# Kernel optimization log

Hardware: AMD Instinct MI355X
Metric: run time of the kernel (lower is better)

The kernel has to match this reference:

```python
import jax, jax.numpy as jnp
import numpy as np

EPS = 1e-5
H, DH = 8, 8  # n_head, d_hidden


def setup_inputs() -> dict:
    key = jax.random.key(0)
    ks = jax.random.split(key, 6)
    B, N, L, D = 1, 512, 1024, 64
    s = 1.0 / np.sqrt(D)
    return {
        "msa": jax.random.normal(ks[0], (B, N, L, D), jnp.float32),
        "ln_w": jnp.ones((D,), jnp.float32),
        "ln_b": jnp.zeros((D,), jnp.float32),
        "Wq": jax.random.normal(ks[1], (D, H * DH), jnp.float32) * s,
        "Wk": jax.random.normal(ks[2], (D, DH), jnp.float32) * s,
        "Wv": jax.random.normal(ks[3], (D, DH), jnp.float32) * s,
        "Wg": jax.random.normal(ks[4], (D, H * DH), jnp.float32) * s,
        "bg": jnp.ones((H * DH,), jnp.float32),
        "Wout": jax.random.normal(ks[5], (D, D), jnp.float32) * s,
        "bout": jnp.zeros((D,), jnp.float32),
    }


def reference(msa, ln_w, ln_b, Wq, Wk, Wv, Wg, bg, Wout, bout):
    B, N, L, D = msa.shape
    # LayerNorm over d_msa
    mu = jnp.mean(msa, axis=-1, keepdims=True)
    var = jnp.mean(jnp.square(msa - mu), axis=-1, keepdims=True)
    x = (msa - mu) * jax.lax.rsqrt(var + EPS) * ln_w + ln_b

    # Global query: project, split heads, mean over the N (sequence) axis
    q = (x @ Wq).reshape(B, N, L, H, DH).mean(axis=1)  # (B, L, H, DH)
    k = x @ Wk  # (B, N, L, DH)
    v = x @ Wv  # (B, N, L, DH)
    gate = jax.nn.sigmoid(x @ Wg + bg)  # (B, N, L, H*DH)

    scale = 1.0 / np.sqrt(DH)
    # SDPA batched over (B, L): q_len = H, kv_len = N, head_dim = DH
    scores = jnp.einsum("blhd,bnld->blhn", q, k) * scale
    attn = jax.nn.softmax(scores, axis=-1)
    o = jnp.einsum("blhn,bnld->blhd", attn, v)  # (B, L, H, DH)
    o = o.reshape(B, 1, L, H * DH)  # broadcast over N via gate

    out = (gate * o) @ Wout + bout  # (B, N, L, D)
    return out
```

## Files before the change

### kernel.cpp

```cpp
#include <hip/hip_runtime.h>
#include <math.h>

#define DD 64
#define NN 512
#define LL 1024
#define EPSF 1e-5f
#define NCH 32

typedef short short8 __attribute__((ext_vector_type(8)));
typedef float f32x4 __attribute__((ext_vector_type(4)));

static __device__ __forceinline__ unsigned bf16_rne(float f) {
  unsigned u = __float_as_uint(f);
  return (u + 0x7FFFu + ((u >> 16) & 1u)) >> 16;
}
static __device__ __forceinline__ float bf16_hi_f(float f) {
  unsigned u = __float_as_uint(f);
  return __uint_as_float((u + 0x7FFFu + ((u >> 16) & 1u)) & 0xFFFF0000u);
}

__global__ __launch_bounds__(256) void kW(const float* __restrict__ Wg,
                                          const float* __restrict__ Wout,
                                          unsigned* __restrict__ Bpk)
{
  const int idx = blockIdx.x * 256 + threadIdx.x;
  const int e2   = idx & 3;
  const int lane = (idx >> 2) & 63;
  const int ctkt = (idx >> 8) & 7;
  const int h    = (idx >> 11) & 1;
  const int mv   = (idx >> 12) & 1;
  const int col  = ((ctkt >> 1) << 4) | (lane & 15);
  const int k0   = ((ctkt & 1) << 5) + ((lane >> 4) << 3) + (e2 << 1);
  const float* W = mv ? Wout : Wg;
  const float w0 = W[k0 * DD + col];
  const float w1 = W[(k0 + 1) * DD + col];
  unsigned b0, b1;
  if (h == 0) { b0 = bf16_rne(w0); b1 = bf16_rne(w1); }
  else        { b0 = bf16_rne(w0 - bf16_hi_f(w0)); b1 = bf16_rne(w1 - bf16_hi_f(w1)); }
  Bpk[idx] = b0 | (b1 << 16);
}

__global__ __launch_bounds__(256, 4) void kA(
    const float* __restrict__ msa, const float* __restrict__ lnw, const float* __restrict__ lnb,
    const float* __restrict__ Wk, const float* __restrict__ Wv,
    float* __restrict__ kb, float* __restrict__ vb, float* __restrict__ xbarP)
{
  __shared__ float xc[4][16][68];
  const int t = threadIdx.x;
  const int lane = t & 63;
  const int w = t >> 6;
  const int l_loc = t & 15;
  const int n_loc = t >> 4;
  const int lt = blockIdx.x & 63;
  const int nc = blockIdx.x >> 6;
  const int l0 = lt * 16;
  const int n = nc * 16 + n_loc;
  const int l = l0 + l_loc;

  float X[DD];
  {
    const float4* rp = (const float4*)(msa + ((size_t)n * LL + l) * DD);
#pragma unroll
    for (int i = 0; i < 16; ++i) {
      const float4 f = rp[i];
      X[4*i+0] = f.x; X[4*i+1] = f.y; X[4*i+2] = f.z; X[4*i+3] = f.w;
    }
  }

  float s = 0.f, s2 = 0.f;
#pragma unroll
  for (int d = 0; d < DD; ++d) { s += X[d]; s2 = fmaf(X[d], X[d], s2); }
  const float mu = s * (1.f / DD);
  const float rs = rsqrtf(fmaf(-mu, mu, s2 * (1.f / DD)) + EPSF);

  float ka[8], va[8];
#pragma unroll
  for (int j = 0; j < 8; ++j) { ka[j] = 0.f; va[j] = 0.f; }
#pragma unroll
  for (int d = 0; d < DD; ++d) {
    const float xn = fmaf((X[d] - mu) * rs, lnw[d], lnb[d]);
    X[d] = xn;
#pragma unroll
    for (int j = 0; j < 8; ++j) {
      ka[j] = fmaf(xn, Wk[d * 8 + j], ka[j]);
      va[j] = fmaf(xn, Wv[d * 8 + j], va[j]);
    }
  }

  {
    float4* kp = (float4*)(kb + ((size_t)l * NN + n) * 8);
    float4* vp = (float4*)(vb + ((size_t)l * NN + n) * 8);
    kp[0] = make_float4(ka[0], ka[1], ka[2], ka[3]);
    kp[1] = make_float4(ka[4], ka[5], ka[6], ka[7]);
    vp[0] = make_float4(va[0], va[1], va[2], va[3]);
    vp[1] = make_float4(va[4], va[5], va[6], va[7]);
  }

  {
    const bool hi1 = (lane & 16) != 0;
#pragma unroll
    for (int k = 0; k < 32; ++k) {
      const float keep = hi1 ? X[k + 32] : X[k];
      const float send = hi1 ? X[k] : X[k + 32];
      X[k] = keep + __shfl_xor(send, 16);
    }
    const bool hi2 = (lane & 32) != 0;
#pragma unroll
    for (int k = 0; k < 16; ++k) {
      const float keep = hi2 ? X[k + 16] : X[k];
      const float send = hi2 ? X[k] : X[k + 16];
      X[k] = keep + __shfl_xor(send, 32);
    }
  }
  const int d0 = ((lane >> 4) & 1) * 32 + (lane >> 5) * 16;
#pragma unroll
  for (int k = 0; k < 16; ++k) xc[w][l_loc][d0 + k] = X[k];
  __syncthreads();

#pragma unroll
  for (int j = 0; j < 4; ++j) {
    const int c = t * 4 + j;
    const int ll = c >> 6, d = c & 63;
    const float sv = xc[0][ll][d] + xc[1][ll][d] + xc[2][ll][d] + xc[3][ll][d];
    xbarP[((size_t)(l0 + ll) * NCH + nc) * DD + d] = sv;
  }
}

__global__ __launch_bounds__(512) void kB(
    const float* __restrict__ kb, const float* __restrict__ vb,
    const float* __restrict__ xbarP, const float* __restrict__ Wq,
    float* __restrict__ ob)
{
  __shared__ float xbL[DD];
  __shared__ float qs[DD];
  __shared__ float ks[NN * 9];
  __shared__ float vs[NN * 9];
  const int l = blockIdx.x;
  const int t = threadIdx.x;
  const int h = t >> 6;
  const int lane = t & 63;

  const float* kl = kb + (size_t)l * NN * 8;
  const float* vl = vb + (size_t)l * NN * 8;
#pragma unroll
  for (int i = 0; i < 8; ++i) {
    const int idx = i * 512 + t;
    const int n = idx >> 3, j = idx & 7;
    ks[n*9 + j] = kl[idx];
    vs[n*9 + j] = vl[idx];
  }
  if (t < DD) {
    float s = 0.f;
    for (int p = 0; p < NCH; ++p) s += xbarP[((size_t)l * NCH + p) * DD + t];
    xbL[t] = s * (1.f / NN);
  }
  __syncthreads();
  if (t < DD) {
    float acc = 0.f;
    for (int d = 0; d < DD; ++d) acc = fmaf(xbL[d], Wq[d*DD + t], acc);
    qs[t] = acc * 0.35355339059327373f;
  }
  __syncthreads();

  float sc[8];
  float m = -1e30f;
#pragma unroll
  for (int i = 0; i < 8; ++i) {
    const int n = i * 64 + lane;
    float s = 0.f;
#pragma unroll
    for (int d = 0; d < 8; ++d) s = fmaf(qs[h*8 + d], ks[n*9 + d], s);
    sc[i] = s;
    m = fmaxf(m, s);
  }
#pragma unroll
  for (int off = 32; off; off >>= 1) m = fmaxf(m, __shfl_xor(m, off));
  float ssum = 0.f;
#pragma unroll
  for (int i = 0; i < 8; ++i) { sc[i] = __expf(sc[i] - m); ssum += sc[i]; }
#pragma unroll
  for (int off = 32; off; off >>= 1) ssum += __shfl_xor(ssum, off);
  const float inv = 1.f / ssum;

  float oacc[8];
#pragma unroll
  for (int d = 0; d < 8; ++d) oacc[d] = 0.f;
#pragma unroll
  for (int i = 0; i < 8; ++i) {
    const int n = i * 64 + lane;
#pragma unroll
    for (int d = 0; d < 8; ++d) oacc[d] = fmaf(sc[i], vs[n*9 + d], oacc[d]);
  }
#pragma unroll
  for (int d = 0; d < 8; ++d) {
#pragma unroll
    for (int off = 32; off; off >>= 1) oacc[d] += __shfl_xor(oacc[d], off);
  }
  if (lane == 0) {
    float4* op = (float4*)(ob + (size_t)l * DD + h * 8);
    op[0] = make_float4(oacc[0]*inv, oacc[1]*inv, oacc[2]*inv, oacc[3]*inv);
    op[1] = make_float4(oacc[4]*inv, oacc[5]*inv, oacc[6]*inv, oacc[7]*inv);
  }
}

__global__ __launch_bounds__(256, 4) void kC(
    const float* __restrict__ msa, const float* __restrict__ lnw, const float* __restrict__ lnb,
    const unsigned* __restrict__ Bpk, const float* __restrict__ bg,
    const float* __restrict__ ob, const float* __restrict__ bout,
    float* __restrict__ out)
{
  __shared__ unsigned Bl[4096];
  __shared__ unsigned short XH[128 * 72];
  __shared__ unsigned short XL[128 * 72];
  const int t = threadIdx.x;
  const int lane = t & 63;
  const int w = t >> 6;
  const int rbase = 32 * w;
  const size_t R0 = (size_t)blockIdx.x * 128;

#pragma unroll
  for (int i = 0; i < 16; ++i) Bl[i * 256 + t] = Bpk[i * 256 + t];

  if (t < 128) {
    const float4* rp = (const float4*)(msa + (R0 + t) * DD);
    float4 r4[16];
#pragma unroll
    for (int i = 0; i < 16; ++i) r4[i] = rp[i];
    float s = 0.f, s2 = 0.f;
#pragma unroll
    for (int i = 0; i < 16; ++i) {
      const float4 f = r4[i];
      s += (f.x + f.y) + (f.z + f.w);
      s2 = fmaf(f.x, f.x, s2); s2 = fmaf(f.y, f.y, s2);
      s2 = fmaf(f.z, f.z, s2); s2 = fmaf(f.w, f.w, s2);
    }
    const float mu = s * (1.f / DD);
    const float rs = rsqrtf(fmaf(-mu, mu, s2 * (1.f / DD)) + EPSF);
    const float aa = rs, bb = -mu * rs;
#pragma unroll
    for (int i = 0; i < 16; ++i) {
      const float xs0 = r4[i].x, xs1 = r4[i].y, xs2 = r4[i].z, xs3 = r4[i].w;
      unsigned hh[4], ll[4];
#define XN_SPLIT(c, xv)                                               \
      {                                                               \
        const int d = 4 * i + (c);                                    \
        const float xn = fmaf(fmaf((xv), aa, bb), lnw[d], lnb[d]);    \
        const float hf = bf16_hi_f(xn);                               \
        hh[c] = bf16_rne(xn);                                         \
        ll[c] = bf16_rne(xn - hf);                                    \
      }
      XN_SPLIT(0, xs0) XN_SPLIT(1, xs1) XN_SPLIT(2, xs2) XN_SPLIT(3, xs3)
#undef XN_SPLIT
      *(uint2*)&XH[t * 72 + 4 * i] = make_uint2(hh[0] | (hh[1] << 16), hh[2] | (hh[3] << 16));
      *(uint2*)&XL[t * 72 + 4 * i] = make_uint2(ll[0] | (ll[1] << 16), ll[2] | (ll[3] << 16));
    }
  }
  __syncthreads();

  auto run_mv = [&](f32x4 acc[2][4]) {
#pragma unroll
    for (int rt = 0; rt < 2; ++rt) {
      const int row = rbase + rt * 16 + (lane & 15);
      const int kg = (lane >> 4) * 8;
      const short8 ah0 = *(const short8*)&XH[row * 72 + kg];
      const short8 ah1 = *(const short8*)&XH[row * 72 + 32 + kg];
      const short8 al0 = *(const short8*)&XL[row * 72 + kg];
      const short8 al1 = *(const short8*)&XL[row * 72 + 32 + kg];
#pragma unroll
      for (int ct = 0; ct < 4; ++ct) {
        const short8 bh0 = *(const short8*)&Bl[((0 * 8 + ct * 2 + 0) * 64 + lane) * 4];
        const short8 bh1 = *(const short8*)&Bl[((0 * 8 + ct * 2 + 1) * 64 + lane) * 4];
        const short8 bl0 = *(const short8*)&Bl[((1 * 8 + ct * 2 + 0) * 64 + lane) * 4];
        const short8 bl1 = *(const short8*)&Bl[((1 * 8 + ct * 2 + 1) * 64 + lane) * 4];
        f32x4 c = acc[rt][ct];
        c = __builtin_amdgcn_mfma_f32_16x16x32_bf16(ah0, bh0, c, 0, 0, 0);
        c = __builtin_amdgcn_mfma_f32_16x16x32_bf16(ah1, bh1, c, 0, 0, 0);
        c = __builtin_amdgcn_mfma_f32_16x16x32_bf16(ah0, bl0, c, 0, 0, 0);
        c = __builtin_amdgcn_mfma_f32_16x16x32_bf16(ah1, bl1, c, 0, 0, 0);
        c = __builtin_amdgcn_mfma_f32_16x16x32_bf16(al0, bh0, c, 0, 0, 0);
        c = __builtin_amdgcn_mfma_f32_16x16x32_bf16(al1, bh1, c, 0, 0, 0);
        acc[rt][ct] = c;
      }
    }
  };

  f32x4 acc[2][4];
#pragma unroll
  for (int rt = 0; rt < 2; ++rt)
#pragma unroll
    for (int ct = 0; ct < 4; ++ct) acc[rt][ct] = f32x4{0.f, 0.f, 0.f, 0.f};
  run_mv(acc);

#pragma unroll
  for (int rt = 0; rt < 2; ++rt) {
    const int rl0 = rbase + rt * 16 + ((lane >> 4) << 2);
#pragma unroll
    for (int ct = 0; ct < 4; ++ct) {
      const int col = ct * 16 + (lane & 15);
      const float bgc = bg[col];
#pragma unroll
      for (int j = 0; j < 4; ++j) {
        const int rl = rl0 + j;
        const int li = (int)((R0 + rl) & (LL - 1));
        const float o = ob[(size_t)li * DD + col];
        const float pre = acc[rt][ct][j] + bgc;
        const float tv = o / (1.f + __expf(-pre));
        const float hf = bf16_hi_f(tv);
        XH[rl * 72 + col] = (unsigned short)bf16_rne(tv);
        XL[rl * 72 + col] = (unsigned short)bf16_rne(tv - hf);
      }
    }
  }
  __syncthreads();

#pragma unroll
  for (int i = 0; i < 16; ++i) Bl[i * 256 + t] = Bpk[4096 + i * 256 + t];
  __syncthreads();

#pragma unroll
  for (int rt = 0; rt < 2; ++rt)
#pragma unroll
    for (int ct = 0; ct < 4; ++ct) {
      const float bo = bout[ct * 16 + (lane & 15)];
      acc[rt][ct] = f32x4{bo, bo, bo, bo};
    }
  run_mv(acc);

#pragma unroll
  for (int rt = 0; rt < 2; ++rt) {
#pragma unroll
    for (int j = 0; j < 4; ++j) {
      const size_t rg = R0 + rbase + rt * 16 + ((lane >> 4) << 2) + j;
#pragma unroll
      for (int ct = 0; ct < 4; ++ct)
        out[rg * DD + ct * 16 + (lane & 15)] = acc[rt][ct][j];
    }
  }
}

extern "C" void kernel_launch(void* const* d_in, const int* in_sizes, int n_in,
                              void* d_out, int out_size, void* d_ws, size_t ws_size,
                              hipStream_t stream)
{
  const float* msa  = (const float*)d_in[0];
  const float* lnw  = (const float*)d_in[1];
  const float* lnb  = (const float*)d_in[2];
  const float* Wq   = (const float*)d_in[3];
  const float* Wk   = (const float*)d_in[4];
  const float* Wv   = (const float*)d_in[5];
  const float* Wg   = (const float*)d_in[6];
  const float* bg   = (const float*)d_in[7];
  const float* Wout = (const float*)d_in[8];
  const float* bout = (const float*)d_in[9];
  float* out = (float*)d_out;

  float* kb    = (float*)d_ws;
  float* vb    = kb + (size_t)LL * NN * 8;
  float* xbarP = vb + (size_t)LL * NN * 8;
  float* ob    = xbarP + (size_t)LL * NCH * DD;
  unsigned* Bpk = (unsigned*)(ob + (size_t)LL * DD);

  kW<<<32, 256, 0, stream>>>(Wg, Wout, Bpk);
  kA<<<64 * NCH, 256, 0, stream>>>(msa, lnw, lnb, Wk, Wv, kb, vb, xbarP);
  kB<<<LL, 512, 0, stream>>>(kb, vb, xbarP, Wq, ob);
  kC<<<(NN * LL) / 128, 256, 0, stream>>>(msa, lnw, lnb, Bpk, bg, ob, bout, out);
}
```

Before: 141.6 us.

## Drop LDS weight staging and block barriers in gated output kernel

The fused gate/output kernel now reads packed bf16 weight fragments straight from global memory (cached) instead of staging them in shared memory. That removes the 16 KB LDS buffer and all three block-wide barriers, since each wave only touches its own rows of the normalized-activation tile. LayerNorm is split across all 256 threads, two per row, combined with a shuffle. The attention output is stored transposed so each lane gets its four row values with one float4 load, and the MFMA loop is reordered so each weight fragment is reused across both row tiles. The risks are more global/L1 traffic for weight fragments and reliance on wave-local LDS ordering for correctness.

Result: faster. 134.1 us (-5.3%).

```diff
diff --git a/kernel.cpp b/kernel.cpp
--- a/kernel.cpp
+++ b/kernel.cpp
@@ -129,7 +129,7 @@
 __global__ __launch_bounds__(512) void kB(
     const float* __restrict__ kb, const float* __restrict__ vb,
     const float* __restrict__ xbarP, const float* __restrict__ Wq,
-    float* __restrict__ ob)
+    float* __restrict__ obT)
 {
   __shared__ float xbL[DD];
   __shared__ float qs[DD];
@@ -197,19 +197,18 @@
     for (int off = 32; off; off >>= 1) oacc[d] += __shfl_xor(oacc[d], off);
   }
   if (lane == 0) {
-    float4* op = (float4*)(ob + (size_t)l * DD + h * 8);
-    op[0] = make_float4(oacc[0]*inv, oacc[1]*inv, oacc[2]*inv, oacc[3]*inv);
-    op[1] = make_float4(oacc[4]*inv, oacc[5]*inv, oacc[6]*inv, oacc[7]*inv);
+#pragma unroll
+    for (int d = 0; d < 8; ++d)
+      obT[(size_t)(h * 8 + d) * LL + l] = oacc[d] * inv;
   }
 }
 
 __global__ __launch_bounds__(256, 4) void kC(
     const float* __restrict__ msa, const float* __restrict__ lnw, const float* __restrict__ lnb,
     const unsigned* __restrict__ Bpk, const float* __restrict__ bg,
-    const float* __restrict__ ob, const float* __restrict__ bout,
+    const float* __restrict__ obT, const float* __restrict__ bout,
     float* __restrict__ out)
 {
-  __shared__ unsigned Bl[4096];
   __shared__ unsigned short XH[128 * 72];
   __shared__ unsigned short XL[128 * 72];
   const int t = threadIdx.x;
@@ -217,33 +216,34 @@
   const int w = t >> 6;
   const int rbase = 32 * w;
   const size_t R0 = (size_t)blockIdx.x * 128;
-
-#pragma unroll
-  for (int i = 0; i < 16; ++i) Bl[i * 256 + t] = Bpk[i * 256 + t];
-
-  if (t < 128) {
-    const float4* rp = (const float4*)(msa + (R0 + t) * DD);
-    float4 r4[16];
-#pragma unroll
-    for (int i = 0; i < 16; ++i) r4[i] = rp[i];
+  const int row = t >> 1;
+  const int half = t & 1;
+
+  {
+    const float4* rp = (const float4*)(msa + (R0 + row) * DD + half * 32);
+    float4 r4[8];
+#pragma unroll
+    for (int i = 0; i < 8; ++i) r4[i] = rp[i];
     float s = 0.f, s2 = 0.f;
 #pragma unroll
-    for (int i = 0; i < 16; ++i) {
+    for (int i = 0; i < 8; ++i) {
       const float4 f = r4[i];
       s += (f.x + f.y) + (f.z + f.w);
       s2 = fmaf(f.x, f.x, s2); s2 = fmaf(f.y, f.y, s2);
       s2 = fmaf(f.z, f.z, s2); s2 = fmaf(f.w, f.w, s2);
     }
+    s += __shfl_xor(s, 1);
+    s2 += __shfl_xor(s2, 1);
     const float mu = s * (1.f / DD);
     const float rs = rsqrtf(fmaf(-mu, mu, s2 * (1.f / DD)) + EPSF);
     const float aa = rs, bb = -mu * rs;
 #pragma unroll
-    for (int i = 0; i < 16; ++i) {
+    for (int i = 0; i < 8; ++i) {
       const float xs0 = r4[i].x, xs1 = r4[i].y, xs2 = r4[i].z, xs3 = r4[i].w;
       unsigned hh[4], ll[4];
 #define XN_SPLIT(c, xv)                                               \
       {                                                               \
-        const int d = 4 * i + (c);                                    \
+        const int d = half * 32 + 4 * i + (c);                        \
         const float xn = fmaf(fmaf((xv), aa, bb), lnw[d], lnb[d]);    \
         const float hf = bf16_hi_f(xn);                               \
         hh[c] = bf16_rne(xn);                                         \
@@ -251,34 +251,41 @@
       }
       XN_SPLIT(0, xs0) XN_SPLIT(1, xs1) XN_SPLIT(2, xs2) XN_SPLIT(3, xs3)
 #undef XN_SPLIT
-      *(uint2*)&XH[t * 72 + 4 * i] = make_uint2(hh[0] | (hh[1] << 16), hh[2] | (hh[3] << 16));
-      *(uint2*)&XL[t * 72 + 4 * i] = make_uint2(ll[0] | (ll[1] << 16), ll[2] | (ll[3] << 16));
-    }
-  }
-  __syncthreads();
-
-  auto run_mv = [&](f32x4 acc[2][4]) {
+      *(uint2*)&XH[row * 72 + half * 32 + 4 * i] =
+          make_uint2(hh[0] | (hh[1] << 16), hh[2] | (hh[3] << 16));
+      *(uint2*)&XL[row * 72 + half * 32 + 4 * i] =
+          make_uint2(ll[0] | (ll[1] << 16), ll[2] | (ll[3] << 16));
+    }
+  }
+
+  const short8* Bp = (const short8*)Bpk;
+
+  auto run_mv = [&](int mvsel, f32x4 acc[2][4]) {
+    short8 ah[2][2], al[2][2];
 #pragma unroll
     for (int rt = 0; rt < 2; ++rt) {
-      const int row = rbase + rt * 16 + (lane & 15);
+      const int ar = rbase + rt * 16 + (lane & 15);
       const int kg = (lane >> 4) * 8;
-      const short8 ah0 = *(const short8*)&XH[row * 72 + kg];
-      const short8 ah1 = *(const short8*)&XH[row * 72 + 32 + kg];
-      const short8 al0 = *(const short8*)&XL[row * 72 + kg];
-      const short8 al1 = *(const short8*)&XL[row * 72 + 32 + kg];
-#pragma unroll
-      for (int ct = 0; ct < 4; ++ct) {
-        const short8 bh0 = *(const short8*)&Bl[((0 * 8 + ct * 2 + 0) * 64 + lane) * 4];
-        const short8 bh1 = *(const short8*)&Bl[((0 * 8 + ct * 2 + 1) * 64 + lane) * 4];
-        const short8 bl0 = *(const short8*)&Bl[((1 * 8 + ct * 2 + 0) * 64 + lane) * 4];
-        const short8 bl1 = *(const short8*)&Bl[((1 * 8 + ct * 2 + 1) * 64 + lane) * 4];
+      ah[rt][0] = *(const short8*)&XH[ar * 72 + kg];
+      ah[rt][1] = *(const short8*)&XH[ar * 72 + 32 + kg];
+      al[rt][0] = *(const short8*)&XL[ar * 72 + kg];
+      al[rt][1] = *(const short8*)&XL[ar * 72 + 32 + kg];
+    }
+#pragma unroll
+    for (int ct = 0; ct < 4; ++ct) {
+      const short8 bh0 = Bp[((mvsel * 2 + 0) * 8 + ct * 2 + 0) * 64 + lane];
+      const short8 bh1 = Bp[((mvsel * 2 + 0) * 8 + ct * 2 + 1) * 64 + lane];
+      const short8 bl0 = Bp[((mvsel * 2 + 1) * 8 + ct * 2 + 0) * 64 + lane];
+      const short8 bl1 = Bp[((mvsel * 2 + 1) * 8 + ct * 2 + 1) * 64 + lane];
+#pragma unroll
+      for (int rt = 0; rt < 2; ++rt) {
         f32x4 c = acc[rt][ct];
-        c = __builtin_amdgcn_mfma_f32_16x16x32_bf16(ah0, bh0, c, 0, 0, 0);
-        c = __builtin_amdgcn_mfma_f32_16x16x32_bf16(ah1, bh1, c, 0, 0, 0);
-        c = __builtin_amdgcn_mfma_f32_16x16x32_bf16(ah0, bl0, c, 0, 0, 0);
-        c = __builtin_amdgcn_mfma_f32_16x16x32_bf16(ah1, bl1, c, 0, 0, 0);
-        c = __builtin_amdgcn_mfma_f32_16x16x32_bf16(al0, bh0, c, 0, 0, 0);
-        c = __builtin_amdgcn_mfma_f32_16x16x32_bf16(al1, bh1, c, 0, 0, 0);
+        c = __builtin_amdgcn_mfma_f32_16x16x32_bf16(ah[rt][0], bh0, c, 0, 0, 0);
+        c = __builtin_amdgcn_mfma_f32_16x16x32_bf16(ah[rt][1], bh1, c, 0, 0, 0);
+        c = __builtin_amdgcn_mfma_f32_16x16x32_bf16(ah[rt][0], bl0, c, 0, 0, 0);
+        c = __builtin_amdgcn_mfma_f32_16x16x32_bf16(ah[rt][1], bl1, c, 0, 0, 0);
+        c = __builtin_amdgcn_mfma_f32_16x16x32_bf16(al[rt][0], bh0, c, 0, 0, 0);
+        c = __builtin_amdgcn_mfma_f32_16x16x32_bf16(al[rt][1], bh1, c, 0, 0, 0);
         acc[rt][ct] = c;
       }
     }
@@ -289,33 +296,30 @@
   for (int rt = 0; rt < 2; ++rt)
 #pragma unroll
     for (int ct = 0; ct < 4; ++ct) acc[rt][ct] = f32x4{0.f, 0.f, 0.f, 0.f};
-  run_mv(acc);
+  run_mv(0, acc);
 
 #pragma unroll
   for (int rt = 0; rt < 2; ++rt) {
     const int rl0 = rbase + rt * 16 + ((lane >> 4) << 2);
+    const int li0 = (int)((R0 + rl0) & (LL - 1));
 #pragma unroll
     for (int ct = 0; ct < 4; ++ct) {
       const int col = ct * 16 + (lane & 15);
+      const float4 ov = *(const float4*)&obT[(size_t)col * LL + li0];
       const float bgc = bg[col];
-#pragma unroll
-      for (int j = 0; j < 4; ++j) {
-        const int rl = rl0 + j;
-        const int li = (int)((R0 + rl) & (LL - 1));
-        const float o = ob[(size_t)li * DD + col];
-        const float pre = acc[rt][ct][j] + bgc;
-        const float tv = o / (1.f + __expf(-pre));
-        const float hf = bf16_hi_f(tv);
-        XH[rl * 72 + col] = (unsigned short)bf16_rne(tv);
-        XL[rl * 72 + col] = (unsigned short)bf16_rne(tv - hf);
+      const float o0 = ov.x, o1 = ov.y, o2 = ov.z, o3 = ov.w;
+#define SIG_STORE(j, ocomp)                                           \
+      {                                                               \
+        const float pre = acc[rt][ct][j] + bgc;                       \
+        const float tv = (ocomp) / (1.f + __expf(-pre));              \
+        const float hf = bf16_hi_f(tv);                               \
+        XH[(rl0 + (j)) * 72 + col] = (unsigned short)bf16_rne(tv);    \
+        XL[(rl0 + (j)) * 72 + col] = (unsigned short)bf16_rne(tv - hf); \
       }
-    }
-  }
-  __syncthreads();
-
-#pragma unroll
-  for (int i = 0; i < 16; ++i) Bl[i * 256 + t] = Bpk[4096 + i * 256 + t];
-  __syncthreads();
+      SIG_STORE(0, o0) SIG_STORE(1, o1) SIG_STORE(2, o2) SIG_STORE(3, o3)
+#undef SIG_STORE
+    }
+  }
 
 #pragma unroll
   for (int rt = 0; rt < 2; ++rt)
@@ -324,7 +328,7 @@
       const float bo = bout[ct * 16 + (lane & 15)];
       acc[rt][ct] = f32x4{bo, bo, bo, bo};
     }
-  run_mv(acc);
+  run_mv(1, acc);
 
 #pragma unroll
   for (int rt = 0; rt < 2; ++rt) {
@@ -357,11 +361,11 @@
   float* kb    = (float*)d_ws;
   float* vb    = kb + (size_t)LL * NN * 8;
   float* xbarP = vb + (size_t)LL * NN * 8;
-  float* ob    = xbarP + (size_t)LL * NCH * DD;
-  unsigned* Bpk = (unsigned*)(ob + (size_t)LL * DD);
+  float* obT   = xbarP + (size_t)LL * NCH * DD;
+  unsigned* Bpk = (unsigned*)(obT + (size_t)DD * LL);
 
   kW<<<32, 256, 0, stream>>>(Wg, Wout, Bpk);
   kA<<<64 * NCH, 256, 0, stream>>>(msa, lnw, lnb, Wk, Wv, kb, vb, xbarP);
-  kB<<<LL, 512, 0, stream>>>(kb, vb, xbarP, Wq, ob);
-  kC<<<(NN * LL) / 128, 256, 0, stream>>>(msa, lnw, lnb, Bpk, bg, ob, bout, out);
-}
+  kB<<<LL, 512, 0, stream>>>(kb, vb, xbarP, Wq, obT);
+  kC<<<(NN * LL) / 128, 256, 0, stream>>>(msa, lnw, lnb, Bpk, bg, obT, bout, out);
+}
```
